# Kernel optimization log

Measured on AMD Instinct MI355X. Metric: run time of the kernel, lower is better.

The kernel has to match this reference:

```python
import jax, jax.numpy as jnp
import numpy as np

B, N, D, K = 16, 512, 256, 12  # batch, nodes, node_dim, num edge types (4 arg + 4 arg' + punct +/- + no_edges +/-)
ITERATION_STEPS = 1


def setup_inputs() -> dict:
    key = jax.random.key(0)
    ks = jax.random.split(key, 8)
    node = jax.random.normal(ks[0], (B, N, D), dtype=jnp.float32)
    node_mask = jax.random.randint(ks[1], (B, N), 0, 2, dtype=jnp.int32)
    graphs = jax.random.randint(ks[2], (K, B, N, N), 0, 2, dtype=jnp.int32)
    s = 1.0 / np.sqrt(D)
    Ww = jax.random.normal(ks[3], (1, D), dtype=jnp.float32) * s   # _node_weight_fc
    bw = jnp.zeros((1,), dtype=jnp.float32)
    Ws = jax.random.normal(ks[4], (D, D), dtype=jnp.float32) * s   # _self_node_fc
    bs = jnp.zeros((D,), dtype=jnp.float32)
    Wk = jax.random.normal(ks[5], (K, D, D), dtype=jnp.float32) * s  # 12 bias-free per-edge-type linears
    return {"node": node, "Ww": Ww, "bw": bw, "Ws": Ws, "bs": bs, "Wk": Wk,
            "node_mask": node_mask, "graphs": graphs}


def reference(node, Ww, bw, Ws, bs, Wk, node_mask, graphs):
    dt = node.dtype
    mask = node_mask.astype(dt)
    eye = jnp.eye(N, dtype=dt)
    # dd_graph = mask_row * mask_col * (1 - diag)
    dd = mask[:, None, :] * mask[:, :, None] * (1.0 - eye)          # [B,N,N]
    g = dd[None] * graphs.astype(dt)                                # [K,B,N,N] masked adjacencies
    neigh = g.sum(axis=(0, 3))                                      # [B,N] total neighbor count
    neigh = jnp.where(neigh >= 1, neigh, jnp.ones((), dt))

    all_w = []
    for _ in range(ITERATION_STEPS):
        # (1) node relatedness
        w = jax.nn.sigmoid(node @ Ww.T + bw)[..., 0]                # [B,N]
        all_w.append(w)
        self_info = node @ Ws.T + bs                                # [B,N,D]
        # (2) message propagation for all 12 edge types, batched
        trans = jnp.einsum('bnd,ked->kbne', node, Wk)               # [K,B,N,D] per-type linear (x @ W.T)
        wg = w[None, :, None, :] * g                                # [K,B,N,N] masked node weights
        agg = jnp.einsum('kbmn,kbnd->bmd', wg, trans) / neigh[..., None]
        # (3) update
        node = jax.nn.relu(self_info + agg)

    all_weight = jnp.stack(all_w, axis=1)                           # [B,steps,N]
    return node, all_weight
```

## Files before the change

### kernel.cpp

```cpp
#include <hip/hip_runtime.h>
#include <hip/hip_bf16.h>
#include <math.h>

#define BB 16
#define NN 512
#define DD 256
#define KK 12

typedef __bf16 bf16x8 __attribute__((ext_vector_type(8)));
typedef __bf16 bf16x4 __attribute__((ext_vector_type(4)));
typedef float  f32x4  __attribute__((ext_vector_type(4)));

#define WS_WM     0
#define WS_NCNT   32768
#define WS_MASKBF 65536
#define WS_NODEBF 81920
#define WS_NODET  4276224
#define WS_WKBF   8470528
#define WS_WSBF   10043392
#define WS_T      10174464

__global__ __launch_bounds__(256) void k1_prep(const float* __restrict__ node,
        const float* __restrict__ Ww, const float* __restrict__ bw,
        const int* __restrict__ node_mask,
        float* __restrict__ wm, __bf16* __restrict__ maskbf,
        __bf16* __restrict__ node_bf, float* __restrict__ all_w) {
    int t = threadIdx.x;
    int lane = t & 63;
    int row = blockIdx.x * 4 + (t >> 6);
    const float4 nv = *(const float4*)(node + (size_t)row * DD + lane * 4);
    const float4 wv = *(const float4*)(Ww + lane * 4);
    float dot = nv.x*wv.x + nv.y*wv.y + nv.z*wv.z + nv.w*wv.w;
    #pragma unroll
    for (int off = 32; off > 0; off >>= 1) dot += __shfl_xor(dot, off);
    float w = 1.0f / (1.0f + expf(-(dot + bw[0])));
    int mk = node_mask[row];
    if (lane == 0) {
        wm[row]     = w * (float)mk;
        all_w[row]  = w;
        maskbf[row] = (__bf16)(float)mk;
    }
    bf16x4 nb = {(__bf16)nv.x, (__bf16)nv.y, (__bf16)nv.z, (__bf16)nv.w};
    *(bf16x4*)(node_bf + (size_t)row * DD + lane * 4) = nb;
}

__global__ __launch_bounds__(256) void k1b_convert(const float* __restrict__ Wk,
        const float* __restrict__ Ws, __bf16* __restrict__ Wk_bf, __bf16* __restrict__ Ws_bf) {
    const int KDD = KK * DD * DD;
    int idx = (blockIdx.x * 256 + threadIdx.x) * 4;
    if (idx < KDD) {
        float4 v = *(const float4*)(Wk + idx);
        bf16x4 o = {(__bf16)v.x, (__bf16)v.y, (__bf16)v.z, (__bf16)v.w};
        *(bf16x4*)(Wk_bf + idx) = o;
    } else {
        int j = idx - KDD;
        if (j < DD * DD) {
            float4 v = *(const float4*)(Ws + j);
            bf16x4 o = {(__bf16)v.x, (__bf16)v.y, (__bf16)v.z, (__bf16)v.w};
            *(bf16x4*)(Ws_bf + j) = o;
        }
    }
}

__global__ __launch_bounds__(256) void k2_transpose(const float* __restrict__ node,
        const float* __restrict__ wm, __bf16* __restrict__ dst) {
    __shared__ float tile[64][65];
    int bx = blockIdx.x;
    int b = bx >> 5; int rest = bx & 31; int nt = rest >> 2; int dt = rest & 3;
    int n0 = nt * 64, d0 = dt * 64;
    int t = threadIdx.x;
    #pragma unroll
    for (int i = 0; i < 16; i++) {
        int idx = i * 256 + t;
        int n = idx >> 6, d = idx & 63;
        tile[n][d] = node[((size_t)(b * NN + n0 + n)) * DD + d0 + d];
    }
    __syncthreads();
    #pragma unroll
    for (int i = 0; i < 16; i++) {
        int idx = i * 256 + t;
        int d = idx >> 6, n = idx & 63;
        float w = wm[b * NN + n0 + n];
        dst[((size_t)(b * DD + d0 + d)) * NN + n0 + n] = (__bf16)(tile[n][d] * w);
    }
}

__global__ __launch_bounds__(256) void k4_stageA(const int* __restrict__ graphs,
        const __bf16* __restrict__ maskbf, const __bf16* __restrict__ node_t,
        __bf16* __restrict__ T, int* __restrict__ ncnt) {
    __shared__ __align__(16) __bf16 Abf[64][520];
    __shared__ float cntp[4][64];
    int bx = blockIdx.x;
    int b  = bx & 15;
    int mt = (bx >> 4) & 7;
    int k  = bx >> 7;
    int m0 = mt * 64;
    int t = threadIdx.x;
    int lane = t & 63;
    int wave = t >> 6;
    int q = lane >> 4;
    int l16 = lane & 15;
    int e0 = wave * 64;

    const int4* gbase = (const int4*)(graphs + ((size_t)((k * BB + b) * NN + m0)) * NN);
    int colbase = (t * 4) & 511;
    int rowpar  = t >> 7;
    #pragma unroll
    for (int jj = 0; jj < 4; jj++) {
        int4 g[8];
        #pragma unroll
        for (int u = 0; u < 8; u++)
            g[u] = gbase[(jj * 8 + u) * 256 + t];
        #pragma unroll
        for (int u = 0; u < 8; u++) {
            int row = 2 * (jj * 8 + u) + rowpar;
            unsigned p0 = (unsigned)g[u].x | ((unsigned)g[u].y << 16);
            unsigned p1 = (unsigned)g[u].z | ((unsigned)g[u].w << 16);
            unsigned drel = (unsigned)(m0 + row - colbase);
            if (drel < 2u)      p0 &= ~(0xFFFFu << (16 * drel));
            else if (drel < 4u) p1 &= ~(0xFFFFu << (16 * (drel - 2)));
            uint2 st; st.x = p0 * 0x3F80u; st.y = p1 * 0x3F80u;
            *(uint2*)&Abf[row][colbase] = st;
        }
    }
    __syncthreads();

    f32x4 acc[4][4];
    #pragma unroll
    for (int i = 0; i < 4; i++)
        #pragma unroll
        for (int j = 0; j < 4; j++) acc[i][j] = (f32x4){0.f, 0.f, 0.f, 0.f};
    f32x4 accC[4];
    #pragma unroll
    for (int i = 0; i < 4; i++) accC[i] = (f32x4){0.f, 0.f, 0.f, 0.f};
    int cw0 = wave * 4;

    #pragma unroll
    for (int kk = 0; kk < 16; kk++) {
        int n0c = kk * 32;
        bf16x8 af[4], bfr[4];
        #pragma unroll
        for (int fm = 0; fm < 4; fm++)
            af[fm] = *(const bf16x8*)&Abf[fm * 16 + l16][n0c + q * 8];
        #pragma unroll
        for (int fd = 0; fd < 4; fd++)
            bfr[fd] = *(const bf16x8*)(node_t +
                ((size_t)(b * DD + e0 + fd * 16 + l16)) * NN + n0c + q * 8);
        #pragma unroll
        for (int fm = 0; fm < 4; fm++)
            #pragma unroll
            for (int fd = 0; fd < 4; fd++)
                acc[fm][fd] = __builtin_amdgcn_mfma_f32_16x16x32_bf16(
                    af[fm], bfr[fd], acc[fm][fd], 0, 0, 0);
        if (kk >= cw0 && kk < cw0 + 4) {
            bf16x8 bfm = (bf16x8){0,0,0,0,0,0,0,0};
            if (l16 == 0)
                bfm = *(const bf16x8*)(maskbf + b * NN + n0c + q * 8);
            #pragma unroll
            for (int fm = 0; fm < 4; fm++)
                accC[fm] = __builtin_amdgcn_mfma_f32_16x16x32_bf16(
                    af[fm], bfm, accC[fm], 0, 0, 0);
        }
    }

    if (l16 == 0) {
        #pragma unroll
        for (int fm = 0; fm < 4; fm++)
            #pragma unroll
            for (int r = 0; r < 4; r++)
                cntp[wave][fm * 16 + q * 4 + r] = accC[fm][r];
    }
    __syncthreads();
    if (t < 64) {
        float c = cntp[0][t] + cntp[1][t] + cntp[2][t] + cntp[3][t];
        atomicAdd(&ncnt[b * NN + m0 + t], (int)(c + 0.5f));
    }

    #pragma unroll
    for (int fm = 0; fm < 4; fm++)
        #pragma unroll
        for (int fd = 0; fd < 4; fd++) {
            int col = e0 + fd * 16 + l16;
            #pragma unroll
            for (int r = 0; r < 4; r++) {
                int m = m0 + fm * 16 + q * 4 + r;
                T[((size_t)((b * NN + m) * KK + k)) * DD + col] = (__bf16)acc[fm][fd][r];
            }
        }
}

__global__ __launch_bounds__(256) void k5_stageB(const __bf16* __restrict__ T,
        const __bf16* __restrict__ Wk_bf, const __bf16* __restrict__ node_bf,
        const __bf16* __restrict__ Ws_bf, const float* __restrict__ bs,
        const int* __restrict__ ncnt, const int* __restrict__ node_mask,
        float* __restrict__ out) {
    __shared__ float redbuf[64][65];
    int bx = blockIdx.x;
    int b = bx & 15;
    int mt = (bx >> 4) & 7;
    int dt = bx >> 7;
    int m0 = mt * 64, d0 = dt * 64;
    int t = threadIdx.x;
    int lane = t & 63;
    int wave = t >> 6;
    int q = lane >> 4;
    int l16 = lane & 15;
    int ew = wave * 64;

    f32x4 acc[4][4];
    #pragma unroll
    for (int i = 0; i < 4; i++)
        #pragma unroll
        for (int j = 0; j < 4; j++) acc[i][j] = (f32x4){0.f, 0.f, 0.f, 0.f};

    for (int k = 0; k < KK; k++) {
        #pragma unroll
        for (int kk = 0; kk < 2; kk++) {
            int eoff = ew + kk * 32 + q * 8;
            bf16x8 af[4], bfr[4];
            #pragma unroll
            for (int fm = 0; fm < 4; fm++)
                af[fm] = *(const bf16x8*)(T +
                    ((size_t)(b * NN + m0 + fm * 16 + l16)) * (KK * DD) + k * DD + eoff);
            #pragma unroll
            for (int fd = 0; fd < 4; fd++)
                bfr[fd] = *(const bf16x8*)(Wk_bf +
                    ((size_t)(k * DD + d0 + fd * 16 + l16)) * DD + eoff);
            #pragma unroll
            for (int fm = 0; fm < 4; fm++)
                #pragma unroll
                for (int fd = 0; fd < 4; fd++)
                    acc[fm][fd] = __builtin_amdgcn_mfma_f32_16x16x32_bf16(
                        af[fm], bfr[fd], acc[fm][fd], 0, 0, 0);
        }
    }

    #pragma unroll
    for (int fm = 0; fm < 4; fm++) {
        #pragma unroll
        for (int r = 0; r < 4; r++) {
            int m = m0 + fm * 16 + q * 4 + r;
            int c = ncnt[b * NN + m];
            float s = (float)node_mask[b * NN + m] / (float)(c >= 1 ? c : 1);
            #pragma unroll
            for (int fd = 0; fd < 4; fd++) acc[fm][fd][r] *= s;
        }
    }

    #pragma unroll
    for (int kk = 0; kk < 2; kk++) {
        int eoff = ew + kk * 32 + q * 8;
        bf16x8 af[4], bfr[4];
        #pragma unroll
        for (int fm = 0; fm < 4; fm++)
            af[fm] = *(const bf16x8*)(node_bf +
                ((size_t)(b * NN + m0 + fm * 16 + l16)) * DD + eoff);
        #pragma unroll
        for (int fd = 0; fd < 4; fd++)
            bfr[fd] = *(const bf16x8*)(Ws_bf +
                ((size_t)(d0 + fd * 16 + l16)) * DD + eoff);
        #pragma unroll
        for (int fm = 0; fm < 4; fm++)
            #pragma unroll
            for (int fd = 0; fd < 4; fd++)
                acc[fm][fd] = __builtin_amdgcn_mfma_f32_16x16x32_bf16(
                    af[fm], bfr[fd], acc[fm][fd], 0, 0, 0);
    }

    for (int w = 0; w < 4; w++) {
        if (wave == w) {
            #pragma unroll
            for (int fm = 0; fm < 4; fm++)
                #pragma unroll
                for (int fd = 0; fd < 4; fd++) {
                    int dd2 = fd * 16 + l16;
                    #pragma unroll
                    for (int r = 0; r < 4; r++) {
                        int mm = fm * 16 + q * 4 + r;
                        if (w == 0) redbuf[mm][dd2] = acc[fm][fd][r];
                        else        redbuf[mm][dd2] += acc[fm][fd][r];
                    }
                }
        }
        __syncthreads();
    }

    int row = t >> 2;
    int c0 = (t & 3) * 16;
    #pragma unroll
    for (int j = 0; j < 4; j++) {
        int d = d0 + c0 + j * 4;
        float4 bv = *(const float4*)(bs + d);
        float4 v;
        v.x = fmaxf(redbuf[row][c0 + j * 4 + 0] + bv.x, 0.0f);
        v.y = fmaxf(redbuf[row][c0 + j * 4 + 1] + bv.y, 0.0f);
        v.z = fmaxf(redbuf[row][c0 + j * 4 + 2] + bv.z, 0.0f);
        v.w = fmaxf(redbuf[row][c0 + j * 4 + 3] + bv.w, 0.0f);
        *(float4*)(out + ((size_t)(b * NN + m0 + row)) * DD + d) = v;
    }
}

extern "C" void kernel_launch(void* const* d_in, const int* in_sizes, int n_in,
                              void* d_out, int out_size, void* d_ws, size_t ws_size,
                              hipStream_t stream) {
    const float* node      = (const float*)d_in[0];
    const float* Ww        = (const float*)d_in[1];
    const float* bw        = (const float*)d_in[2];
    const float* Ws        = (const float*)d_in[3];
    const float* bs        = (const float*)d_in[4];
    const float* Wk        = (const float*)d_in[5];
    const int*   node_mask = (const int*)d_in[6];
    const int*   graphs    = (const int*)d_in[7];
    float* out   = (float*)d_out;
    float* all_w = out + (size_t)BB * NN * DD;

    char* ws = (char*)d_ws;
    float*  wm      = (float*)(ws + WS_WM);
    int*    ncnt    = (int*)(ws + WS_NCNT);
    __bf16* maskbf  = (__bf16*)(ws + WS_MASKBF);
    __bf16* node_bf = (__bf16*)(ws + WS_NODEBF);
    __bf16* node_t  = (__bf16*)(ws + WS_NODET);
    __bf16* Wk_bf   = (__bf16*)(ws + WS_WKBF);
    __bf16* Ws_bf   = (__bf16*)(ws + WS_WSBF);
    __bf16* Tbuf    = (__bf16*)(ws + WS_T);

    hipMemsetAsync(ncnt, 0, BB * NN * sizeof(int), stream);
    k1_prep    <<<2048, 256, 0, stream>>>(node, Ww, bw, node_mask, wm, maskbf, node_bf, all_w);
    k1b_convert<<< 832, 256, 0, stream>>>(Wk, Ws, Wk_bf, Ws_bf);
    k2_transpose<<<512, 256, 0, stream>>>(node, wm, node_t);
    k4_stageA  <<<1536, 256, 0, stream>>>(graphs, maskbf, node_t, Tbuf, ncnt);
    k5_stageB  <<< 512, 256, 0, stream>>>(Tbuf, Wk_bf, node_bf, Ws_bf, bs, ncnt, node_mask, out);
}
```

Baseline: 405.2 us.

## Fuse adjacency aggregation and per-type projection into one kernel with LDS intermediate

Merges the two GEMM stages into a single kernel. Each block handles 32 rows of one batch, loops over the 12 edge types, and keeps the aggregated intermediate T in shared memory instead of writing it to global memory. The next edge type's graph tile is prefetched into registers while the current one is being computed. Neighbor counts are accumulated in-block, which removes the atomic, the memset and the T round trip. The cost is only 256 blocks of 512 threads, so parallelism is lower, and the serial k loop needs extra barriers.

```diff
diff --git a/kernel.cpp b/kernel.cpp
--- a/kernel.cpp
+++ b/kernel.cpp
@@ -12,13 +12,11 @@
 typedef float  f32x4  __attribute__((ext_vector_type(4)));
 
 #define WS_WM     0
-#define WS_NCNT   32768
-#define WS_MASKBF 65536
-#define WS_NODEBF 81920
-#define WS_NODET  4276224
-#define WS_WKBF   8470528
-#define WS_WSBF   10043392
-#define WS_T      10174464
+#define WS_MASKBF 32768
+#define WS_NODEBF 49152
+#define WS_NODET  4243456
+#define WS_WKBF   8437760
+#define WS_WSBF   10010624
 
 __global__ __launch_bounds__(256) void k1_prep(const float* __restrict__ node,
         const float* __restrict__ Ww, const float* __restrict__ bw,
@@ -85,219 +83,187 @@
     }
 }
 
-__global__ __launch_bounds__(256) void k4_stageA(const int* __restrict__ graphs,
-        const __bf16* __restrict__ maskbf, const __bf16* __restrict__ node_t,
-        __bf16* __restrict__ T, int* __restrict__ ncnt) {
-    __shared__ __align__(16) __bf16 Abf[64][520];
-    __shared__ float cntp[4][64];
+__global__ __launch_bounds__(512, 2) void k45_fused(const int* __restrict__ graphs,
+        const int* __restrict__ node_mask, const __bf16* __restrict__ maskbf,
+        const __bf16* __restrict__ node_t, const __bf16* __restrict__ node_bf,
+        const __bf16* __restrict__ Wk_bf, const __bf16* __restrict__ Ws_bf,
+        const float* __restrict__ bs, float* __restrict__ out) {
+    __shared__ __align__(16) __bf16 Abf[32][520];
+    __shared__ __align__(16) __bf16 Tk[32][264];
+    __shared__ float cntp[8][32];
+    __shared__ float sm[32];
     int bx = blockIdx.x;
-    int b  = bx & 15;
-    int mt = (bx >> 4) & 7;
-    int k  = bx >> 7;
-    int m0 = mt * 64;
+    int b  = (bx & 7) + 8 * ((bx >> 3) & 1);
+    int mt = bx >> 4;
+    int m0 = mt * 32;
     int t = threadIdx.x;
     int lane = t & 63;
-    int wave = t >> 6;
+    int w = t >> 6;
     int q = lane >> 4;
     int l16 = lane & 15;
-    int e0 = wave * 64;
-
-    const int4* gbase = (const int4*)(graphs + ((size_t)((k * BB + b) * NN + m0)) * NN);
-    int colbase = (t * 4) & 511;
-    int rowpar  = t >> 7;
-    #pragma unroll
-    for (int jj = 0; jj < 4; jj++) {
-        int4 g[8];
-        #pragma unroll
-        for (int u = 0; u < 8; u++)
-            g[u] = gbase[(jj * 8 + u) * 256 + t];
+    int esub = w * 32;
+    int dsub = w * 32;
+
+    int crow = t >> 7;
+    int ccol = (t & 127) * 4;
+
+    f32x4 accO[2][2];
+    #pragma unroll
+    for (int i = 0; i < 2; i++)
+        #pragma unroll
+        for (int j = 0; j < 2; j++) accO[i][j] = (f32x4){0.f, 0.f, 0.f, 0.f};
+    f32x4 accC[2];
+    accC[0] = (f32x4){0.f, 0.f, 0.f, 0.f};
+    accC[1] = (f32x4){0.f, 0.f, 0.f, 0.f};
+
+    int4 g[8];
+    {
+        const int4* gb = (const int4*)(graphs + ((size_t)(b * NN + m0)) * NN);
+        #pragma unroll
+        for (int u = 0; u < 8; u++) g[u] = gb[u * 512 + t];
+    }
+
+    #pragma unroll 1
+    for (int k = 0; k < KK; k++) {
         #pragma unroll
         for (int u = 0; u < 8; u++) {
-            int row = 2 * (jj * 8 + u) + rowpar;
+            int row = u * 4 + crow;
             unsigned p0 = (unsigned)g[u].x | ((unsigned)g[u].y << 16);
             unsigned p1 = (unsigned)g[u].z | ((unsigned)g[u].w << 16);
-            unsigned drel = (unsigned)(m0 + row - colbase);
+            unsigned drel = (unsigned)(m0 + row - ccol);
             if (drel < 2u)      p0 &= ~(0xFFFFu << (16 * drel));
             else if (drel < 4u) p1 &= ~(0xFFFFu << (16 * (drel - 2)));
             uint2 st; st.x = p0 * 0x3F80u; st.y = p1 * 0x3F80u;
-            *(uint2*)&Abf[row][colbase] = st;
-        }
+            *(uint2*)&Abf[row][ccol] = st;
+        }
+        __syncthreads();
+
+        if (k < KK - 1) {
+            const int4* gb = (const int4*)(graphs + ((size_t)(((k + 1) * BB + b) * NN + m0)) * NN);
+            #pragma unroll
+            for (int u = 0; u < 8; u++) g[u] = gb[u * 512 + t];
+        }
+
+        f32x4 accT[2][2];
+        #pragma unroll
+        for (int i = 0; i < 2; i++)
+            #pragma unroll
+            for (int j = 0; j < 2; j++) accT[i][j] = (f32x4){0.f, 0.f, 0.f, 0.f};
+        #pragma unroll
+        for (int kk = 0; kk < 16; kk++) {
+            int n0c = kk * 32;
+            bf16x8 af[2], bfr[2];
+            #pragma unroll
+            for (int fm = 0; fm < 2; fm++)
+                af[fm] = *(const bf16x8*)&Abf[fm * 16 + l16][n0c + q * 8];
+            #pragma unroll
+            for (int fd = 0; fd < 2; fd++)
+                bfr[fd] = *(const bf16x8*)(node_t +
+                    ((size_t)(b * DD + esub + fd * 16 + l16)) * NN + n0c + q * 8);
+            #pragma unroll
+            for (int fm = 0; fm < 2; fm++)
+                #pragma unroll
+                for (int fd = 0; fd < 2; fd++)
+                    accT[fm][fd] = __builtin_amdgcn_mfma_f32_16x16x32_bf16(
+                        af[fm], bfr[fd], accT[fm][fd], 0, 0, 0);
+            if ((kk >> 1) == w) {
+                bf16x8 bfm = (bf16x8){0,0,0,0,0,0,0,0};
+                if (l16 == 0)
+                    bfm = *(const bf16x8*)(maskbf + b * NN + n0c + q * 8);
+                accC[0] = __builtin_amdgcn_mfma_f32_16x16x32_bf16(af[0], bfm, accC[0], 0, 0, 0);
+                accC[1] = __builtin_amdgcn_mfma_f32_16x16x32_bf16(af[1], bfm, accC[1], 0, 0, 0);
+            }
+        }
+        #pragma unroll
+        for (int fm = 0; fm < 2; fm++)
+            #pragma unroll
+            for (int fd = 0; fd < 2; fd++) {
+                int col = esub + fd * 16 + l16;
+                #pragma unroll
+                for (int r = 0; r < 4; r++)
+                    Tk[fm * 16 + q * 4 + r][col] = (__bf16)accT[fm][fd][r];
+            }
+        __syncthreads();
+
+        #pragma unroll
+        for (int ee = 0; ee < 8; ee++) {
+            int e0c = ee * 32;
+            bf16x8 afT[2], bw2[2];
+            #pragma unroll
+            for (int fm = 0; fm < 2; fm++)
+                afT[fm] = *(const bf16x8*)&Tk[fm * 16 + l16][e0c + q * 8];
+            #pragma unroll
+            for (int fd = 0; fd < 2; fd++)
+                bw2[fd] = *(const bf16x8*)(Wk_bf +
+                    ((size_t)(k * DD + dsub + fd * 16 + l16)) * DD + e0c + q * 8);
+            #pragma unroll
+            for (int fm = 0; fm < 2; fm++)
+                #pragma unroll
+                for (int fd = 0; fd < 2; fd++)
+                    accO[fm][fd] = __builtin_amdgcn_mfma_f32_16x16x32_bf16(
+                        afT[fm], bw2[fd], accO[fm][fd], 0, 0, 0);
+        }
+    }
+
+    if (l16 == 0) {
+        #pragma unroll
+        for (int fm = 0; fm < 2; fm++)
+            #pragma unroll
+            for (int r = 0; r < 4; r++)
+                cntp[w][fm * 16 + q * 4 + r] = accC[fm][r];
     }
     __syncthreads();
-
-    f32x4 acc[4][4];
-    #pragma unroll
-    for (int i = 0; i < 4; i++)
-        #pragma unroll
-        for (int j = 0; j < 4; j++) acc[i][j] = (f32x4){0.f, 0.f, 0.f, 0.f};
-    f32x4 accC[4];
-    #pragma unroll
-    for (int i = 0; i < 4; i++) accC[i] = (f32x4){0.f, 0.f, 0.f, 0.f};
-    int cw0 = wave * 4;
-
-    #pragma unroll
-    for (int kk = 0; kk < 16; kk++) {
-        int n0c = kk * 32;
-        bf16x8 af[4], bfr[4];
-        #pragma unroll
-        for (int fm = 0; fm < 4; fm++)
-            af[fm] = *(const bf16x8*)&Abf[fm * 16 + l16][n0c + q * 8];
-        #pragma unroll
-        for (int fd = 0; fd < 4; fd++)
-            bfr[fd] = *(const bf16x8*)(node_t +
-                ((size_t)(b * DD + e0 + fd * 16 + l16)) * NN + n0c + q * 8);
-        #pragma unroll
-        for (int fm = 0; fm < 4; fm++)
-            #pragma unroll
-            for (int fd = 0; fd < 4; fd++)
-                acc[fm][fd] = __builtin_amdgcn_mfma_f32_16x16x32_bf16(
-                    af[fm], bfr[fd], acc[fm][fd], 0, 0, 0);
-        if (kk >= cw0 && kk < cw0 + 4) {
-            bf16x8 bfm = (bf16x8){0,0,0,0,0,0,0,0};
-            if (l16 == 0)
-                bfm = *(const bf16x8*)(maskbf + b * NN + n0c + q * 8);
-            #pragma unroll
-            for (int fm = 0; fm < 4; fm++)
-                accC[fm] = __builtin_amdgcn_mfma_f32_16x16x32_bf16(
-                    af[fm], bfm, accC[fm], 0, 0, 0);
-        }
-    }
-
-    if (l16 == 0) {
-        #pragma unroll
-        for (int fm = 0; fm < 4; fm++)
-            #pragma unroll
-            for (int r = 0; r < 4; r++)
-                cntp[wave][fm * 16 + q * 4 + r] = accC[fm][r];
+    if (t < 32) {
+        float c = 0.0f;
+        #pragma unroll
+        for (int w8 = 0; w8 < 8; w8++) c += cntp[w8][t];
+        int mk = node_mask[b * NN + m0 + t];
+        sm[t] = (float)mk / (c >= 0.5f ? c : 1.0f);
     }
     __syncthreads();
-    if (t < 64) {
-        float c = cntp[0][t] + cntp[1][t] + cntp[2][t] + cntp[3][t];
-        atomicAdd(&ncnt[b * NN + m0 + t], (int)(c + 0.5f));
-    }
-
-    #pragma unroll
-    for (int fm = 0; fm < 4; fm++)
-        #pragma unroll
-        for (int fd = 0; fd < 4; fd++) {
-            int col = e0 + fd * 16 + l16;
+
+    #pragma unroll
+    for (int fm = 0; fm < 2; fm++)
+        #pragma unroll
+        for (int r = 0; r < 4; r++) {
+            float s = sm[fm * 16 + q * 4 + r];
+            #pragma unroll
+            for (int fd = 0; fd < 2; fd++) accO[fm][fd][r] *= s;
+        }
+
+    #pragma unroll
+    for (int ee = 0; ee < 8; ee++) {
+        int e0c = ee * 32;
+        bf16x8 afS[2], bwS[2];
+        #pragma unroll
+        for (int fm = 0; fm < 2; fm++)
+            afS[fm] = *(const bf16x8*)(node_bf +
+                ((size_t)(b * NN + m0 + fm * 16 + l16)) * DD + e0c + q * 8);
+        #pragma unroll
+        for (int fd = 0; fd < 2; fd++)
+            bwS[fd] = *(const bf16x8*)(Ws_bf +
+                ((size_t)(dsub + fd * 16 + l16)) * DD + e0c + q * 8);
+        #pragma unroll
+        for (int fm = 0; fm < 2; fm++)
+            #pragma unroll
+            for (int fd = 0; fd < 2; fd++)
+                accO[fm][fd] = __builtin_amdgcn_mfma_f32_16x16x32_bf16(
+                    afS[fm], bwS[fd], accO[fm][fd], 0, 0, 0);
+    }
+
+    #pragma unroll
+    for (int fm = 0; fm < 2; fm++)
+        #pragma unroll
+        for (int fd = 0; fd < 2; fd++) {
+            int d = dsub + fd * 16 + l16;
+            float bsv = bs[d];
             #pragma unroll
             for (int r = 0; r < 4; r++) {
                 int m = m0 + fm * 16 + q * 4 + r;
-                T[((size_t)((b * NN + m) * KK + k)) * DD + col] = (__bf16)acc[fm][fd][r];
+                float v = accO[fm][fd][r] + bsv;
+                out[((size_t)(b * NN + m)) * DD + d] = fmaxf(v, 0.0f);
             }
         }
-}
-
-__global__ __launch_bounds__(256) void k5_stageB(const __bf16* __restrict__ T,
-        const __bf16* __restrict__ Wk_bf, const __bf16* __restrict__ node_bf,
-        const __bf16* __restrict__ Ws_bf, const float* __restrict__ bs,
-        const int* __restrict__ ncnt, const int* __restrict__ node_mask,
-        float* __restrict__ out) {
-    __shared__ float redbuf[64][65];
-    int bx = blockIdx.x;
-    int b = bx & 15;
-    int mt = (bx >> 4) & 7;
-    int dt = bx >> 7;
-    int m0 = mt * 64, d0 = dt * 64;
-    int t = threadIdx.x;
-    int lane = t & 63;
-    int wave = t >> 6;
-    int q = lane >> 4;
-    int l16 = lane & 15;
-    int ew = wave * 64;
-
-    f32x4 acc[4][4];
-    #pragma unroll
-    for (int i = 0; i < 4; i++)
-        #pragma unroll
-        for (int j = 0; j < 4; j++) acc[i][j] = (f32x4){0.f, 0.f, 0.f, 0.f};
-
-    for (int k = 0; k < KK; k++) {
-        #pragma unroll
-        for (int kk = 0; kk < 2; kk++) {
-            int eoff = ew + kk * 32 + q * 8;
-            bf16x8 af[4], bfr[4];
-            #pragma unroll
-            for (int fm = 0; fm < 4; fm++)
-                af[fm] = *(const bf16x8*)(T +
-                    ((size_t)(b * NN + m0 + fm * 16 + l16)) * (KK * DD) + k * DD + eoff);
-            #pragma unroll
-            for (int fd = 0; fd < 4; fd++)
-                bfr[fd] = *(const bf16x8*)(Wk_bf +
-                    ((size_t)(k * DD + d0 + fd * 16 + l16)) * DD + eoff);
-            #pragma unroll
-            for (int fm = 0; fm < 4; fm++)
-                #pragma unroll
-                for (int fd = 0; fd < 4; fd++)
-                    acc[fm][fd] = __builtin_amdgcn_mfma_f32_16x16x32_bf16(
-                        af[fm], bfr[fd], acc[fm][fd], 0, 0, 0);
-        }
-    }
-
-    #pragma unroll
-    for (int fm = 0; fm < 4; fm++) {
-        #pragma unroll
-        for (int r = 0; r < 4; r++) {
-            int m = m0 + fm * 16 + q * 4 + r;
-            int c = ncnt[b * NN + m];
-            float s = (float)node_mask[b * NN + m] / (float)(c >= 1 ? c : 1);
-            #pragma unroll
-            for (int fd = 0; fd < 4; fd++) acc[fm][fd][r] *= s;
-        }
-    }
-
-    #pragma unroll
-    for (int kk = 0; kk < 2; kk++) {
-        int eoff = ew + kk * 32 + q * 8;
-        bf16x8 af[4], bfr[4];
-        #pragma unroll
-        for (int fm = 0; fm < 4; fm++)
-            af[fm] = *(const bf16x8*)(node_bf +
-                ((size_t)(b * NN + m0 + fm * 16 + l16)) * DD + eoff);
-        #pragma unroll
-        for (int fd = 0; fd < 4; fd++)
-            bfr[fd] = *(const bf16x8*)(Ws_bf +
-                ((size_t)(d0 + fd * 16 + l16)) * DD + eoff);
-        #pragma unroll
-        for (int fm = 0; fm < 4; fm++)
-            #pragma unroll
-            for (int fd = 0; fd < 4; fd++)
-                acc[fm][fd] = __builtin_amdgcn_mfma_f32_16x16x32_bf16(
-                    af[fm], bfr[fd], acc[fm][fd], 0, 0, 0);
-    }
-
-    for (int w = 0; w < 4; w++) {
-        if (wave == w) {
-            #pragma unroll
-            for (int fm = 0; fm < 4; fm++)
-                #pragma unroll
-                for (int fd = 0; fd < 4; fd++) {
-                    int dd2 = fd * 16 + l16;
-                    #pragma unroll
-                    for (int r = 0; r < 4; r++) {
-                        int mm = fm * 16 + q * 4 + r;
-                        if (w == 0) redbuf[mm][dd2] = acc[fm][fd][r];
-                        else        redbuf[mm][dd2] += acc[fm][fd][r];
-                    }
-                }
-        }
-        __syncthreads();
-    }
-
-    int row = t >> 2;
-    int c0 = (t & 3) * 16;
-    #pragma unroll
-    for (int j = 0; j < 4; j++) {
-        int d = d0 + c0 + j * 4;
-        float4 bv = *(const float4*)(bs + d);
-        float4 v;
-        v.x = fmaxf(redbuf[row][c0 + j * 4 + 0] + bv.x, 0.0f);
-        v.y = fmaxf(redbuf[row][c0 + j * 4 + 1] + bv.y, 0.0f);
-        v.z = fmaxf(redbuf[row][c0 + j * 4 + 2] + bv.z, 0.0f);
-        v.w = fmaxf(redbuf[row][c0 + j * 4 + 3] + bv.w, 0.0f);
-        *(float4*)(out + ((size_t)(b * NN + m0 + row)) * DD + d) = v;
-    }
 }
 
 extern "C" void kernel_launch(void* const* d_in, const int* in_sizes, int n_in,
@@ -316,18 +282,15 @@
 
     char* ws = (char*)d_ws;
     float*  wm      = (float*)(ws + WS_WM);
-    int*    ncnt    = (int*)(ws + WS_NCNT);
     __bf16* maskbf  = (__bf16*)(ws + WS_MASKBF);
     __bf16* node_bf = (__bf16*)(ws + WS_NODEBF);
     __bf16* node_t  = (__bf16*)(ws + WS_NODET);
     __bf16* Wk_bf   = (__bf16*)(ws + WS_WKBF);
     __bf16* Ws_bf   = (__bf16*)(ws + WS_WSBF);
-    __bf16* Tbuf    = (__bf16*)(ws + WS_T);
-
-    hipMemsetAsync(ncnt, 0, BB * NN * sizeof(int), stream);
+
     k1_prep    <<<2048, 256, 0, stream>>>(node, Ww, bw, node_mask, wm, maskbf, node_bf, all_w);
     k1b_convert<<< 832, 256, 0, stream>>>(Wk, Ws, Wk_bf, Ws_bf);
     k2_transpose<<<512, 256, 0, stream>>>(node, wm, node_t);
-    k4_stageA  <<<1536, 256, 0, stream>>>(graphs, maskbf, node_t, Tbuf, ncnt);
-    k5_stageB  <<< 512, 256, 0, stream>>>(Tbuf, Wk_bf, node_bf, Ws_bf, bs, ncnt, node_mask, out);
-}
+    k45_fused  <<< 256, 512, 0, stream>>>(graphs, node_mask, maskbf, node_t, node_bf,
+                                          Wk_bf, Ws_bf, bs, out);
+}
```

Result: faster. 354.8 us (-12.4%).
